# Kernel optimization log

Hardware: AMD Instinct MI355X
Metric: run time of the kernel (lower is better)

Reference implementation:

```python
import jax, jax.numpy as jnp
import numpy as np

N = 100000   # nodes
E = 3200000  # edges (before self-loops)
IN, H, OUT = 128, 256, 40

def glorot(key, shape):
    lim = (6.0 / (shape[0] + shape[1])) ** 0.5
    return jax.random.uniform(key, shape, jnp.float32, -lim, lim)

def setup_inputs() -> dict:
    key = jax.random.key(0)
    ks = jax.random.split(key, 8)
    x = jax.random.normal(ks[0], (N, IN), jnp.float32)
    edge_index = jax.random.randint(ks[1], (2, E), 0, N, dtype=jnp.int32)
    return {
        "x": x,
        "edge_index": edge_index,
        "W0": glorot(ks[2], (IN, H)),  "b0": jnp.zeros((H,), jnp.float32),
        "W1": glorot(ks[3], (H, H)),   "b1": jnp.zeros((H,), jnp.float32),
        "W2": glorot(ks[4], (H, OUT)), "b2": jnp.zeros((OUT,), jnp.float32),
    }

def _gcn_norm(edge_index, n):
    # PyG gcn_norm: add self-loops, symmetric D^{-1/2} A D^{-1/2}
    loops = jnp.arange(n, dtype=edge_index.dtype)
    src = jnp.concatenate([edge_index[0], loops])
    dst = jnp.concatenate([edge_index[1], loops])
    deg = jax.ops.segment_sum(jnp.ones_like(src, jnp.float32), dst, num_segments=n)
    dinv = jnp.where(deg > 0, jax.lax.rsqrt(deg), 0.0)
    norm = dinv[src] * dinv[dst]  # [E+N]
    return src, dst, norm

def _gcn_layer(h, W, b, src, dst, norm, n):
    h = h @ W                                   # transform first (PyG order)
    msg = h[src] * norm[:, None]                # gather + scale
    agg = jax.ops.segment_sum(msg, dst, num_segments=n)  # scatter-add
    return agg + b

def reference(x, edge_index, W0, b0, W1, b1, W2, b2):
    n = x.shape[0]
    src, dst, norm = _gcn_norm(edge_index, n)
    h = jnp.tanh(_gcn_layer(x, W0, b0, src, dst, norm, n))  # dropout = identity (eval)
    h = jnp.tanh(_gcn_layer(h, W1, b1, src, dst, norm, n))
    out = _gcn_layer(h, W2, b2, src, dst, norm, n)
    return jax.nn.log_softmax(out, axis=1)
```

## Files before the change

### kernel.cpp

```cpp
#include <hip/hip_runtime.h>
#include <hip/hip_bf16.h>
#include <cmath>


typedef unsigned short u16;
typedef __attribute__((ext_vector_type(8))) short short8;
typedef __attribute__((ext_vector_type(4))) float f32x4;

#define BSHIFT 10
#define BNODES (1 << BSHIFT)
#define ECAP   36864
#define BMASK 0x00FF00FFu

__device__ __forceinline__ u16 f2bf(float f) {
    unsigned int u = __float_as_uint(f);
    u += 0x7fffu + ((u >> 16) & 1u);
    return (u16)(u >> 16);
}
__device__ __forceinline__ float bflo(unsigned int u) { return __uint_as_float(u << 16); }
__device__ __forceinline__ float bfhi(unsigned int u) { return __uint_as_float(u & 0xffff0000u); }

__device__ __forceinline__ int q8(float v) {
    return (int)rintf(fminf(fmaxf(v, -127.0f), 127.0f));
}


__global__ __launch_bounds__(128) void init_gcur_kernel(
        int* __restrict__ gcur, int nb) {
    int b = blockIdx.x * 128 + threadIdx.x;
    if (b < nb) gcur[b] = b * ECAP;
}

__global__ __launch_bounds__(256) void bucketize_kernel(
        const int* __restrict__ src, const int* __restrict__ dst,
        int* __restrict__ gcur, unsigned int* __restrict__ ebuf, int E) {
    __shared__ int cnt4[4][128];
    __shared__ int base4[4][128];
    int tid = threadIdx.x;
    int set = tid >> 6;
    int e0 = blockIdx.x * 2048;
    int cend = min(e0 + 2048, E);
    for (int i = tid; i < 512; i += 256) ((int*)cnt4)[i] = 0;
    __syncthreads();
    int rank[8], bk[8];
    unsigned int pk[8];
#pragma unroll
    for (int j = 0; j < 8; j++) {
        int e = e0 + j * 256 + tid;
        bk[j] = -1;
        if (e < cend) {
            int d = dst[e];
            bk[j] = d >> BSHIFT;
            pk[j] = (unsigned int)src[e] | ((unsigned int)(d & (BNODES - 1)) << 17);
            rank[j] = atomicAdd(&cnt4[set][bk[j]], 1);
        }
    }
    __syncthreads();
    if (tid < 128) {
        int c0 = cnt4[0][tid], c1 = cnt4[1][tid], c2 = cnt4[2][tid], c3 = cnt4[3][tid];
        int tot = c0 + c1 + c2 + c3;
        int b = (tot > 0) ? atomicAdd(&gcur[tid], tot) : 0;
        base4[0][tid] = b;
        base4[1][tid] = b + c0;
        base4[2][tid] = b + c0 + c1;
        base4[3][tid] = b + c0 + c1 + c2;
    }
    __syncthreads();
#pragma unroll
    for (int j = 0; j < 8; j++)
        if (bk[j] >= 0) ebuf[base4[set][bk[j]] + rank[j]] = pk[j];
}

__global__ __launch_bounds__(256) void deg_hist_kernel(
        const unsigned int* __restrict__ ebuf, const int* __restrict__ gcur,
        int* __restrict__ degi, int N) {
    __shared__ int h[BNODES];
    int b = blockIdx.x;
    int nb0 = b << BSHIFT;
    int nodes = min(BNODES, N - nb0);
    for (int i = threadIdx.x; i < nodes; i += 256) h[i] = 0;
    __syncthreads();
    int estart = b * ECAP;
    int eend = gcur[b];
    for (int e = estart + threadIdx.x; e < eend; e += 256)
        atomicAdd(&h[ebuf[e] >> 17], 1);
    __syncthreads();
    for (int i = threadIdx.x; i < nodes; i += 256) degi[nb0 + i] = h[i];
}

__global__ __launch_bounds__(256) void dinv_kernel(
        const int* __restrict__ degi, float* __restrict__ dinv, int n) {
    int i = blockIdx.x * 256 + threadIdx.x;
    if (i < n) dinv[i] = rsqrtf((float)degi[i] + 1.0f);
}

__global__ __launch_bounds__(256) void scan_part_kernel(
        const int* __restrict__ deg, int* __restrict__ part, int n) {
    __shared__ int s[256];
    int i = blockIdx.x * 256 + threadIdx.x;
    s[threadIdx.x] = (i < n) ? deg[i] : 0;
    __syncthreads();
    for (int off = 128; off; off >>= 1) {
        if (threadIdx.x < off) s[threadIdx.x] += s[threadIdx.x + off];
        __syncthreads();
    }
    if (threadIdx.x == 0) part[blockIdx.x] = s[0];
}

__global__ __launch_bounds__(1024) void scan_top_kernel(
        int* __restrict__ part, int nb) {
    __shared__ int s[1024];
    int t = threadIdx.x;
    int v = (t < nb) ? part[t] : 0;
    s[t] = v;
    __syncthreads();
    for (int off = 1; off < 1024; off <<= 1) {
        int u = (t >= off) ? s[t - off] : 0;
        __syncthreads();
        s[t] += u;
        __syncthreads();
    }
    if (t < nb) part[t] = s[t] - v;
}

__global__ __launch_bounds__(256) void scan_apply_kernel(
        const int* __restrict__ deg, const int* __restrict__ part,
        int* __restrict__ rs, int n) {
    __shared__ int s[256];
    int i = blockIdx.x * 256 + threadIdx.x;
    int v = (i < n) ? deg[i] : 0;
    s[threadIdx.x] = v;
    __syncthreads();
    for (int off = 1; off < 256; off <<= 1) {
        int u = (threadIdx.x >= off) ? s[threadIdx.x - off] : 0;
        __syncthreads();
        s[threadIdx.x] += u;
        __syncthreads();
    }
    if (i < n) rs[i] = part[blockIdx.x] + s[threadIdx.x] - v;
}

__global__ __launch_bounds__(256) void csr_fill_kernel(
        const unsigned int* __restrict__ ebuf, const int* __restrict__ gcur,
        const int* __restrict__ rs, int* __restrict__ csr, int N) {
    __shared__ int lcur[BNODES];
    int b = blockIdx.x;
    int nb0 = b << BSHIFT;
    int nodes = min(BNODES, N - nb0);
    for (int i = threadIdx.x; i < nodes; i += 256) lcur[i] = rs[nb0 + i];
    __syncthreads();
    int estart = b * ECAP;
    int eend = gcur[b];
    for (int e = estart + threadIdx.x; e < eend; e += 256) {
        unsigned int v = ebuf[e];
        int s = v & 0x1FFFF;
        int dl = v >> 17;
        int pos = atomicAdd(&lcur[dl], 1);
        csr[pos] = s;
    }
}

__global__ __launch_bounds__(256) void wt_kernel(
        const float* __restrict__ W, u16* __restrict__ Wt, int K, int NC) {
    int i = blockIdx.x * 256 + threadIdx.x;
    if (i < K * NC) {
        int k = i / NC, c = i % NC;
        Wt[(size_t)c * K + k] = f2bf(W[i]);
    }
}

__global__ __launch_bounds__(256) void scale_x_kernel(
        const float* __restrict__ x, const float* __restrict__ dinv,
        unsigned int* __restrict__ out, int total4) {
    int i = blockIdx.x * 256 + threadIdx.x;
    if (i >= total4) return;
    int n = i >> 5;
    float4 v = reinterpret_cast<const float4*>(x)[i];
    float s = dinv[n] * 63.5f;
    int a0 = q8(v.x * s), a1 = q8(v.y * s), a2 = q8(v.z * s), a3 = q8(v.w * s);
    out[i] = (unsigned int)(a0 & 0xff) | ((unsigned int)(a1 & 0xff) << 8) |
             ((unsigned int)(a2 & 0xff) << 16) | ((unsigned int)(a3 & 0xff) << 24);
}

__global__ __launch_bounds__(256) void agg128_i8_kernel(
        const signed char* __restrict__ in, u16* __restrict__ out,
        const int* __restrict__ rs, const int* __restrict__ deg,
        const int* __restrict__ csr, const float* __restrict__ dinv, int n) {
    int wid = blockIdx.x * 4 + (threadIdx.x >> 6);
    if (wid >= n) return;
    int lane = threadIdx.x & 63;
    int half = lane >> 5;
    int l32 = lane & 31;
    int start = rs[wid];
    int cnt = deg[wid];

    unsigned int ae = 0, ao = 0;
    if (half == 0) {
        unsigned int q = *reinterpret_cast<const unsigned int*>(
            in + (size_t)wid * 128 + l32 * 4) ^ 0x80808080u;
        ae += q & BMASK; ao += (q >> 8) & BMASK;
    }
    int i = 0;
    for (; i + 4 <= cnt; i += 4) {
        int s0 = csr[start + i + half];
        int s1 = csr[start + i + 2 + half];
        unsigned int q0 = *reinterpret_cast<const unsigned int*>(
            in + (size_t)s0 * 128 + l32 * 4) ^ 0x80808080u;
        unsigned int q1 = *reinterpret_cast<const unsigned int*>(
            in + (size_t)s1 * 128 + l32 * 4) ^ 0x80808080u;
        ae += (q0 & BMASK) + (q1 & BMASK);
        ao += ((q0 >> 8) & BMASK) + ((q1 >> 8) & BMASK);
    }
    for (; i + 2 <= cnt; i += 2) {
        int s0 = csr[start + i + half];
        unsigned int q0 = *reinterpret_cast<const unsigned int*>(
            in + (size_t)s0 * 128 + l32 * 4) ^ 0x80808080u;
        ae += q0 & BMASK; ao += (q0 >> 8) & BMASK;
    }
    if (i < cnt && half == 0) {
        int s0 = csr[start + i];
        unsigned int q0 = *reinterpret_cast<const unsigned int*>(
            in + (size_t)s0 * 128 + l32 * 4) ^ 0x80808080u;
        ae += q0 & BMASK; ao += (q0 >> 8) & BMASK;
    }
    ae += (unsigned int)__shfl((int)ae, lane + 32);
    ao += (unsigned int)__shfl((int)ao, lane + 32);
    if (half == 0) {
        int bias = 128 * (cnt + 1);
        float c = dinv[wid] * (2.0f / 127.0f);
        float f0 = (float)((int)(ae & 0xFFFFu) - bias) * c;
        float f1 = (float)((int)(ao & 0xFFFFu) - bias) * c;
        float f2 = (float)((int)(ae >> 16) - bias) * c;
        float f3 = (float)((int)(ao >> 16) - bias) * c;
        uint2 o;
        o.x = (unsigned)f2bf(f0) | ((unsigned)f2bf(f1) << 16);
        o.y = (unsigned)f2bf(f2) | ((unsigned)f2bf(f3) << 16);
        reinterpret_cast<uint2*>(out + (size_t)wid * 128)[l32] = o;
    }
}

__global__ __launch_bounds__(256) void agg_i8_kernel(
        const signed char* __restrict__ in, u16* __restrict__ out,
        const int* __restrict__ rs, const int* __restrict__ deg,
        const int* __restrict__ csr, const float* __restrict__ dinv, int n) {
    int wid = blockIdx.x * 4 + (threadIdx.x >> 6);
    if (wid >= n) return;
    int lane = threadIdx.x & 63;
    int start = rs[wid];
    int cnt = deg[wid];

    unsigned int q = *reinterpret_cast<const unsigned int*>(
        in + (size_t)wid * 256 + lane * 4) ^ 0x80808080u;
    unsigned int ae = q & BMASK, ao = (q >> 8) & BMASK;

    int i = 0;
    for (; i + 4 <= cnt; i += 4) {
        int s0 = csr[start + i];
        int s1 = csr[start + i + 1];
        int s2 = csr[start + i + 2];
        int s3 = csr[start + i + 3];
        unsigned int q0 = *reinterpret_cast<const unsigned int*>(
            in + (size_t)s0 * 256 + lane * 4) ^ 0x80808080u;
        unsigned int q1 = *reinterpret_cast<const unsigned int*>(
            in + (size_t)s1 * 256 + lane * 4) ^ 0x80808080u;
        unsigned int q2 = *reinterpret_cast<const unsigned int*>(
            in + (size_t)s2 * 256 + lane * 4) ^ 0x80808080u;
        unsigned int q3 = *reinterpret_cast<const unsigned int*>(
            in + (size_t)s3 * 256 + lane * 4) ^ 0x80808080u;
        ae += (q0 & BMASK) + (q1 & BMASK) + (q2 & BMASK) + (q3 & BMASK);
        ao += ((q0 >> 8) & BMASK) + ((q1 >> 8) & BMASK) +
              ((q2 >> 8) & BMASK) + ((q3 >> 8) & BMASK);
    }
    for (; i < cnt; i++) {
        int s0 = csr[start + i];
        unsigned int q0 = *reinterpret_cast<const unsigned int*>(
            in + (size_t)s0 * 256 + lane * 4) ^ 0x80808080u;
        ae += q0 & BMASK; ao += (q0 >> 8) & BMASK;
    }
    int bias = 128 * (cnt + 1);
    float c = dinv[wid] * (1.0f / 127.0f);
    float f0 = (float)((int)(ae & 0xFFFFu) - bias) * c;
    float f1 = (float)((int)(ao & 0xFFFFu) - bias) * c;
    float f2 = (float)((int)(ae >> 16) - bias) * c;
    float f3 = (float)((int)(ao >> 16) - bias) * c;
    uint2 o;
    o.x = (unsigned)f2bf(f0) | ((unsigned)f2bf(f1) << 16);
    o.y = (unsigned)f2bf(f2) | ((unsigned)f2bf(f3) << 16);
    reinterpret_cast<uint2*>(out + (size_t)wid * 256)[lane] = o;
}

template<int EPI, typename CT>
__global__ __launch_bounds__(256) void mfma_mm_kernel(
        const u16* __restrict__ A, const u16* __restrict__ Bt,
        CT* __restrict__ C, int M, int K, int NC, int ldc,
        const float* __restrict__ bias, const float* __restrict__ postscale,
        float qs) {
    __shared__ u16 As[128 * 40];
    __shared__ u16 Bs[64 * 40];
    int t = threadIdx.x;
    int w = t >> 6, lane = t & 63, quad = lane >> 4, l16 = lane & 15;
    int row0 = blockIdx.x * 128;
    int col0 = blockIdx.y * 64;

    f32x4 acc[2][4];
#pragma unroll
    for (int s = 0; s < 2; s++)
#pragma unroll
        for (int nb = 0; nb < 4; nb++)
            acc[s][nb] = (f32x4){0.f, 0.f, 0.f, 0.f};

    int bn = t >> 2, bkq = (t & 3) << 3;
    for (int k0 = 0; k0 < K; k0 += 32) {
#pragma unroll
        for (int i = t; i < 512; i += 256) {
            int r = i >> 2, c = (i & 3) << 3;
            int gr = row0 + r;
            uint4 v = {0u, 0u, 0u, 0u};
            if (gr < M)
                v = *reinterpret_cast<const uint4*>(A + (size_t)gr * K + k0 + c);
            *reinterpret_cast<uint4*>(&As[r * 40 + c]) = v;
        }
        {
            int gc = col0 + bn;
            uint4 v = {0u, 0u, 0u, 0u};
            if (gc < NC)
                v = *reinterpret_cast<const uint4*>(Bt + (size_t)gc * K + k0 + bkq);
            *reinterpret_cast<uint4*>(&Bs[bn * 40 + bkq]) = v;
        }
        __syncthreads();

        short8 af[2], bf[4];
        af[0] = *reinterpret_cast<const short8*>(&As[(w * 32 + l16) * 40 + quad * 8]);
        af[1] = *reinterpret_cast<const short8*>(&As[(w * 32 + 16 + l16) * 40 + quad * 8]);
#pragma unroll
        for (int nb = 0; nb < 4; nb++)
            bf[nb] = *reinterpret_cast<const short8*>(&Bs[(nb * 16 + l16) * 40 + quad * 8]);
#pragma unroll
        for (int s = 0; s < 2; s++)
#pragma unroll
            for (int nb = 0; nb < 4; nb++)
                acc[s][nb] = __builtin_amdgcn_mfma_f32_16x16x32_bf16(
                    af[s], bf[nb], acc[s][nb], 0, 0, 0);
        __syncthreads();
    }

#pragma unroll
    for (int s = 0; s < 2; s++) {
        int rbase = row0 + w * 32 + s * 16 + quad * 4;
#pragma unroll
        for (int nb = 0; nb < 4; nb++) {
            int gc = col0 + nb * 16 + l16;
#pragma unroll
            for (int r = 0; r < 4; r++) {
                int gr = rbase + r;
                if (gr >= M || gc >= NC) continue;
                float v = acc[s][nb][r];
                if constexpr (EPI == 1) v = tanhf(v + bias[gc]);
                else                    v = v * postscale[gr];
                if constexpr (sizeof(CT) == 1) {
                    float m = qs;
                    if constexpr (EPI == 1) m *= postscale[gr];
                    C[(size_t)gr * ldc + gc] = (CT)q8(v * m);
                } else {
                    C[(size_t)gr * ldc + gc] = (CT)f2bf(v);
                }
            }
        }
    }
}

__global__ __launch_bounds__(256) void agg40_ls_kernel(
        const signed char* __restrict__ in, const int* __restrict__ rs,
        const int* __restrict__ deg, const int* __restrict__ csr,
        const float* __restrict__ dinv, const float* __restrict__ bias,
        float* __restrict__ out, int n) {
    int wid = blockIdx.x * 4 + (threadIdx.x >> 6);
    if (wid >= n) return;
    int lane = threadIdx.x & 63;
    int grp = lane / 10;
    int col = lane - grp * 10;
    bool act = lane < 60;
    int start = rs[wid];
    int cnt = deg[wid];

    unsigned int ae = 0, ao = 0;
    if (lane < 10) {
        unsigned int q = *reinterpret_cast<const unsigned int*>(
            in + (size_t)wid * 64 + col * 4) ^ 0x80808080u;
        ae += q & BMASK; ao += (q >> 8) & BMASK;
    }
    for (int base = 0; base < cnt; base += 6) {
        int e = base + grp;
        if (act && e < cnt) {
            int s0 = csr[start + e];
            unsigned int q = *reinterpret_cast<const unsigned int*>(
                in + (size_t)s0 * 64 + col * 4) ^ 0x80808080u;
            ae += q & BMASK; ao += (q >> 8) & BMASK;
        }
    }
    ae += (unsigned int)__shfl((int)ae, lane + 30);
    ao += (unsigned int)__shfl((int)ao, lane + 30);
    ae += (unsigned int)__shfl((int)ae, lane + 10) + (unsigned int)__shfl((int)ae, lane + 20);
    ao += (unsigned int)__shfl((int)ao, lane + 10) + (unsigned int)__shfl((int)ao, lane + 20);

    bool act10 = lane < 10;
    float s = dinv[wid];
    float v0 = -INFINITY, v1 = -INFINITY, v2 = -INFINITY, v3 = -INFINITY;
    if (act10) {
        int bb = 128 * (cnt + 1);
        float c = s * (1.0f / 63.0f);
        int cc = lane * 4;
        v0 = (float)((int)(ae & 0xFFFFu) - bb) * c + bias[cc + 0];
        v1 = (float)((int)(ao & 0xFFFFu) - bb) * c + bias[cc + 1];
        v2 = (float)((int)(ae >> 16) - bb) * c + bias[cc + 2];
        v3 = (float)((int)(ao >> 16) - bb) * c + bias[cc + 3];
    }
    float m = fmaxf(fmaxf(v0, v1), fmaxf(v2, v3));
    for (int off = 8; off; off >>= 1) m = fmaxf(m, __shfl_xor(m, off));
    float e = 0.f;
    if (act10) e = __expf(v0 - m) + __expf(v1 - m) + __expf(v2 - m) + __expf(v3 - m);
    for (int off = 8; off; off >>= 1) e += __shfl_xor(e, off);
    float ls = logf(e);
    if (act10) {
        float4 o;
        o.x = v0 - m - ls; o.y = v1 - m - ls; o.z = v2 - m - ls; o.w = v3 - m - ls;
        reinterpret_cast<float4*>(out + (size_t)wid * 40)[lane] = o;
    }
}

extern "C" void kernel_launch(void* const* d_in, const int* in_sizes, int n_in,
                              void* d_out, int out_size, void* d_ws, size_t ws_size,
                              hipStream_t stream) {
    const float* x  = (const float*)d_in[0];
    const int*   ei = (const int*)d_in[1];
    const float* W0 = (const float*)d_in[2];
    const float* b0 = (const float*)d_in[3];
    const float* W1 = (const float*)d_in[4];
    const float* b1 = (const float*)d_in[5];
    const float* W2 = (const float*)d_in[6];
    const float* b2 = (const float*)d_in[7];
    float* out = (float*)d_out;

    const int N = in_sizes[0] / 128;
    const int E = in_sizes[1] / 2;
    const int IN = 128, H = 256, OUT = 40;
    const int NB = (N + BNODES - 1) >> BSHIFT;

    char* p = (char*)d_ws;
    auto carve = [&](size_t bytes) -> void* {
        void* r = (void*)p;
        p += (bytes + 255) & ~(size_t)255;
        return r;
    };
    float*        dinv = (float*)carve((size_t)N * 4);
    int*          degi = (int*)  carve((size_t)N * 4);
    int*          rs   = (int*)  carve((size_t)N * 4);
    int*          part = (int*)  carve((size_t)1024 * 4);
    int*          gcur = (int*)  carve((size_t)128 * 4);
    int*          csr  = (int*)  carve((size_t)E * 4);
    unsigned int* ebuf = (unsigned int*)carve((size_t)NB * ECAP * 4);
    u16*          Wt0  = (u16*)  carve((size_t)IN * H * 2);
    u16*          Wt1  = (u16*)  carve((size_t)H * H * 2);
    u16*          Wt2  = (u16*)  carve((size_t)H * OUT * 2);
    u16*          U1   = (u16*)  carve((size_t)N * H * 2);
    u16*          U2   = (u16*)  carve((size_t)N * H * 2);

    signed char* Xq   = (signed char*)U1;
    u16*         T0bf = U1 + (size_t)N * IN / 2 + 64;
    signed char* H0q  = (signed char*)U2;
    u16*         T1bf = U1;
    u16*         h1bf = U2;
    signed char* G2q  = (signed char*)U1;

    const int* src = ei;
    const int* dst = ei + E;

    int gN = (N + 255) / 256;
    int gW = (N + 3) / 4;
    int gMM = (N + 127) / 128;
    int gA = (E + 2047) / 2048;

    init_gcur_kernel<<<1, 128, 0, stream>>>(gcur, NB);
    bucketize_kernel<<<gA, 256, 0, stream>>>(src, dst, gcur, ebuf, E);
    deg_hist_kernel<<<NB, 256, 0, stream>>>(ebuf, gcur, degi, N);
    dinv_kernel<<<gN, 256, 0, stream>>>(degi, dinv, N);
    scan_part_kernel<<<gN, 256, 0, stream>>>(degi, part, N);
    scan_top_kernel<<<1, 1024, 0, stream>>>(part, gN);
    scan_apply_kernel<<<gN, 256, 0, stream>>>(degi, part, rs, N);
    csr_fill_kernel<<<NB, 256, 0, stream>>>(ebuf, gcur, rs, csr, N);

    wt_kernel<<<(IN * H + 255) / 256, 256, 0, stream>>>(W0, Wt0, IN, H);
    wt_kernel<<<(H * H + 255) / 256, 256, 0, stream>>>(W1, Wt1, H, H);
    wt_kernel<<<(H * OUT + 255) / 256, 256, 0, stream>>>(W2, Wt2, H, OUT);

    int t4x = N * (IN / 4);
    scale_x_kernel<<<(t4x + 255) / 256, 256, 0, stream>>>(
        x, dinv, (unsigned int*)Xq, t4x);
    agg128_i8_kernel<<<gW, 256, 0, stream>>>(Xq, T0bf, rs, degi, csr, dinv, N);
    mfma_mm_kernel<1, signed char><<<dim3(gMM, H / 64), 256, 0, stream>>>(
        T0bf, Wt0, H0q, N, IN, H, H, b0, dinv, 127.0f);

    agg_i8_kernel<<<gW, 256, 0, stream>>>(H0q, T1bf, rs, degi, csr, dinv, N);
    mfma_mm_kernel<1, u16><<<dim3(gMM, H / 64), 256, 0, stream>>>(
        T1bf, Wt1, h1bf, N, H, H, H, b1, nullptr, 0.f);

    mfma_mm_kernel<0, signed char><<<dim3(gMM, 1), 256, 0, stream>>>(
        h1bf, Wt2, G2q, N, H, OUT, 64, nullptr, dinv, 63.0f);
    agg40_ls_kernel<<<gW, 256, 0, stream>>>(G2q, rs, degi, csr, dinv, b2, out, N);
}
```

Baseline: 663.7 us.

## Replace tiled LDS GEMM with full-width register-blocked MFMA for 256-column layers

The 256-column GEMMs for layers 0 and 1 now run in a new kernel where each block covers all 256 output columns. Fragments of A and B are loaded straight from global memory into registers, with no shared-memory staging and no barriers. This reads each A row once instead of once per 64-column tile, and B (the weights) is expected to stay in cache. In exchange the kernel holds 128 accumulator VGPRs per lane, which lowers occupancy, and its B loads are uncoalesced strided reads. The output layer gets a specialised single-tile kernel.

```diff
diff --git a/kernel.cpp b/kernel.cpp
--- a/kernel.cpp
+++ b/kernel.cpp
@@ -290,17 +290,72 @@
 }
 
 template<int EPI, typename CT>
-__global__ __launch_bounds__(256) void mfma_mm_kernel(
+__global__ __launch_bounds__(256) void mm_wide_kernel(
         const u16* __restrict__ A, const u16* __restrict__ Bt,
-        CT* __restrict__ C, int M, int K, int NC, int ldc,
+        CT* __restrict__ C, int M, int K,
         const float* __restrict__ bias, const float* __restrict__ postscale,
         float qs) {
+    int t = threadIdx.x;
+    int w = t >> 6, lane = t & 63, quad = lane >> 4, l16 = lane & 15;
+    int row0 = blockIdx.x * 128;
+
+    int r0 = row0 + w * 32 + l16;
+    int r1 = r0 + 16;
+    int r0c = min(r0, M - 1);
+    int r1c = min(r1, M - 1);
+    const u16* a0p = A + (size_t)r0c * K + quad * 8;
+    const u16* a1p = A + (size_t)r1c * K + quad * 8;
+    const u16* bp  = Bt + (size_t)l16 * K + quad * 8;
+
+    f32x4 acc[2][16];
+#pragma unroll
+    for (int s = 0; s < 2; s++)
+#pragma unroll
+        for (int nb = 0; nb < 16; nb++)
+            acc[s][nb] = (f32x4){0.f, 0.f, 0.f, 0.f};
+
+    for (int k0 = 0; k0 < K; k0 += 32) {
+        short8 af0 = *reinterpret_cast<const short8*>(a0p + k0);
+        short8 af1 = *reinterpret_cast<const short8*>(a1p + k0);
+#pragma unroll
+        for (int nb = 0; nb < 16; nb++) {
+            short8 bf = *reinterpret_cast<const short8*>(bp + (size_t)nb * 16 * K + k0);
+            acc[0][nb] = __builtin_amdgcn_mfma_f32_16x16x32_bf16(af0, bf, acc[0][nb], 0, 0, 0);
+            acc[1][nb] = __builtin_amdgcn_mfma_f32_16x16x32_bf16(af1, bf, acc[1][nb], 0, 0, 0);
+        }
+    }
+
+#pragma unroll
+    for (int s = 0; s < 2; s++) {
+        int rbase = row0 + w * 32 + s * 16 + quad * 4;
+#pragma unroll
+        for (int nb = 0; nb < 16; nb++) {
+            int gc = nb * 16 + l16;
+#pragma unroll
+            for (int r = 0; r < 4; r++) {
+                int gr = rbase + r;
+                if (gr >= M) continue;
+                float v = acc[s][nb][r];
+                if constexpr (EPI == 1) v = tanhf(v + bias[gc]);
+                if constexpr (sizeof(CT) == 1) {
+                    C[(size_t)gr * 256 + gc] = (CT)q8(v * qs * postscale[gr]);
+                } else {
+                    C[(size_t)gr * 256 + gc] = (CT)f2bf(v);
+                }
+            }
+        }
+    }
+}
+
+__global__ __launch_bounds__(256) void mm2_kernel(
+        const u16* __restrict__ A, const u16* __restrict__ Bt,
+        signed char* __restrict__ C, int M, int K, int NC, int ldc,
+        const float* __restrict__ postscale, float qs) {
     __shared__ u16 As[128 * 40];
     __shared__ u16 Bs[64 * 40];
     int t = threadIdx.x;
     int w = t >> 6, lane = t & 63, quad = lane >> 4, l16 = lane & 15;
     int row0 = blockIdx.x * 128;
-    int col0 = blockIdx.y * 64;
 
     f32x4 acc[2][4];
 #pragma unroll
@@ -321,10 +376,9 @@
             *reinterpret_cast<uint4*>(&As[r * 40 + c]) = v;
         }
         {
-            int gc = col0 + bn;
             uint4 v = {0u, 0u, 0u, 0u};
-            if (gc < NC)
-                v = *reinterpret_cast<const uint4*>(Bt + (size_t)gc * K + k0 + bkq);
+            if (bn < NC)
+                v = *reinterpret_cast<const uint4*>(Bt + (size_t)bn * K + k0 + bkq);
             *reinterpret_cast<uint4*>(&Bs[bn * 40 + bkq]) = v;
         }
         __syncthreads();
@@ -349,21 +403,13 @@
         int rbase = row0 + w * 32 + s * 16 + quad * 4;
 #pragma unroll
         for (int nb = 0; nb < 4; nb++) {
-            int gc = col0 + nb * 16 + l16;
+            int gc = nb * 16 + l16;
 #pragma unroll
             for (int r = 0; r < 4; r++) {
                 int gr = rbase + r;
                 if (gr >= M || gc >= NC) continue;
-                float v = acc[s][nb][r];
-                if constexpr (EPI == 1) v = tanhf(v + bias[gc]);
-                else                    v = v * postscale[gr];
-                if constexpr (sizeof(CT) == 1) {
-                    float m = qs;
-                    if constexpr (EPI == 1) m *= postscale[gr];
-                    C[(size_t)gr * ldc + gc] = (CT)q8(v * m);
-                } else {
-                    C[(size_t)gr * ldc + gc] = (CT)f2bf(v);
-                }
+                float v = acc[s][nb][r] * postscale[gr];
+                C[(size_t)gr * ldc + gc] = (signed char)q8(v * qs);
             }
         }
     }
@@ -497,14 +543,14 @@
     scale_x_kernel<<<(t4x + 255) / 256, 256, 0, stream>>>(
         x, dinv, (unsigned int*)Xq, t4x);
     agg128_i8_kernel<<<gW, 256, 0, stream>>>(Xq, T0bf, rs, degi, csr, dinv, N);
-    mfma_mm_kernel<1, signed char><<<dim3(gMM, H / 64), 256, 0, stream>>>(
-        T0bf, Wt0, H0q, N, IN, H, H, b0, dinv, 127.0f);
+    mm_wide_kernel<1, signed char><<<gMM, 256, 0, stream>>>(
+        T0bf, Wt0, H0q, N, IN, b0, dinv, 127.0f);
 
     agg_i8_kernel<<<gW, 256, 0, stream>>>(H0q, T1bf, rs, degi, csr, dinv, N);
-    mfma_mm_kernel<1, u16><<<dim3(gMM, H / 64), 256, 0, stream>>>(
-        T1bf, Wt1, h1bf, N, H, H, H, b1, nullptr, 0.f);
-
-    mfma_mm_kernel<0, signed char><<<dim3(gMM, 1), 256, 0, stream>>>(
-        h1bf, Wt2, G2q, N, H, OUT, 64, nullptr, dinv, 63.0f);
+    mm_wide_kernel<1, u16><<<gMM, 256, 0, stream>>>(
+        T1bf, Wt1, h1bf, N, H, b1, nullptr, 0.f);
+
+    mm2_kernel<<<gMM, 256, 0, stream>>>(
+        h1bf, Wt2, G2q, N, H, OUT, 64, dinv, 63.0f);
     agg40_ls_kernel<<<gW, 256, 0, stream>>>(G2q, rs, degi, csr, dinv, b2, out, N);
 }
```

Measured after the change: 901.4 us. 1.36x slower.
